# Optimization experiments

Measured on AMD Instinct MI355X. Metric: run time of the kernel, lower is better.

The kernel has to match this reference:

```python
import jax, jax.numpy as jnp
import numpy as np

THETA = 10000.0


def apply_rope(t):
    """Partial rotary on first head_dim//2 dims, interleaved pairs (rotary_embedding_torch).
    t: (B, H, S, D) float32."""
    B, H, S, D = t.shape
    rot_dim = D // 2  # RotaryEmbedding(head_dim // 2)
    inv_freq = 1.0 / (THETA ** (jnp.arange(0, rot_dim, 2, dtype=jnp.float32) / rot_dim))  # (rot_dim//2,)
    pos = jnp.arange(S, dtype=jnp.float32)
    freqs = pos[:, None] * inv_freq[None, :]            # (S, rot_dim//2)
    freqs = jnp.repeat(freqs, 2, axis=-1)               # (S, rot_dim) interleaved
    cos, sin = jnp.cos(freqs), jnp.sin(freqs)           # (S, rot_dim)
    t_rot, t_pass = t[..., :rot_dim], t[..., rot_dim:]
    x1 = t_rot[..., 0::2]
    x2 = t_rot[..., 1::2]
    rot_half = jnp.stack((-x2, x1), axis=-1).reshape(t_rot.shape)
    t_rot = t_rot * cos + rot_half * sin
    return jnp.concatenate([t_rot, t_pass], axis=-1)


def setup_inputs() -> dict:
    key = jax.random.key(0)
    k1, k2, k3, k4, k5 = jax.random.split(key, 5)
    B, S, Dm = 2, 2048, 1024
    scale = 1.0 / np.sqrt(Dm)
    return {
        "x": jax.random.normal(k1, (B, S, Dm), dtype=jnp.float32),
        "Wqkv": jax.random.normal(k2, (3 * Dm, Dm), dtype=jnp.float32) * scale,
        "bqkv": jax.random.normal(k3, (3 * Dm,), dtype=jnp.float32) * 0.01,
        "Wout": jax.random.normal(k4, (Dm, Dm), dtype=jnp.float32) * scale,
        "bout": jax.random.normal(k5, (Dm,), dtype=jnp.float32) * 0.01,
    }


def reference(x, Wqkv, bqkv, Wout, bout):
    B, S, Dm = x.shape
    H = 16
    Dh = Dm // H
    qkv = x @ Wqkv.T + bqkv                              # (B, S, 3*Dm)
    qkv = qkv.reshape(B, S, 3, H, Dh).transpose(2, 0, 3, 1, 4)  # (3, B, H, S, Dh)
    q, k, v = qkv[0], qkv[1], qkv[2]
    q = apply_rope(q.astype(jnp.float32))
    k = apply_rope(k.astype(jnp.float32))
    scores = jnp.einsum("bhqd,bhkd->bhqk", q, k) / jnp.sqrt(jnp.float32(Dh))
    attn = jax.nn.softmax(scores, axis=-1)
    out = jnp.einsum("bhqk,bhkd->bhqd", attn, v)         # (B, H, S, Dh)
    out = out.transpose(0, 2, 1, 3).reshape(B, S, Dm)
    return out @ Wout.T + bout
```

## Files before the change

### kernel.cpp

```cpp
#include <hip/hip_runtime.h>

#define S_LEN 2048
#define DMODEL 1024
#define NHEAD 16
#define DHEAD 64
#define BATCH 2
#define BH_TOT (BATCH * NHEAD)
#define TOK (BATCH * S_LEN)
#define NQKV (3 * DMODEL)

#define QSCALE 0.18033688011112042f

typedef float  f32x4  __attribute__((ext_vector_type(4)));
typedef float  f32x16 __attribute__((ext_vector_type(16)));
typedef int    i32x4  __attribute__((ext_vector_type(4)));
typedef __bf16 bf16x8 __attribute__((ext_vector_type(8)));
typedef __bf16 bf16x4 __attribute__((ext_vector_type(4)));
typedef __bf16 bf16x2 __attribute__((ext_vector_type(2)));

typedef __attribute__((address_space(1))) void* as1_ptr;
typedef __attribute__((address_space(3))) void* as3_ptr;

__device__ __forceinline__ void gl2lds16(const void* g, void* l) {
  __builtin_amdgcn_global_load_lds((as1_ptr)(void*)g, (as3_ptr)l, 16, 0, 0);
}

__device__ __forceinline__ f32x4 mfma32(bf16x8 a, bf16x8 b, f32x4 c) {
  return __builtin_amdgcn_mfma_f32_16x16x32_bf16(a, b, c, 0, 0, 0);
}

__device__ __forceinline__ f32x16 mfma3216(bf16x8 a, bf16x8 b, f32x16 c) {
  return __builtin_amdgcn_mfma_f32_32x32x16_bf16(a, b, c, 0, 0, 0);
}

__device__ __forceinline__ unsigned pack2(float a, float b) {
  bf16x2 t;
  t[0] = (__bf16)a;
  t[1] = (__bf16)b;
  return __builtin_bit_cast(unsigned, t);
}

__device__ __forceinline__ bf16x8 pfrag8(int hi,
                                         float a0, float a1, float a2, float a3,
                                         float a4, float a5, float a6, float a7) {
  const unsigned wA = pack2(a0, a1);
  const unsigned wB = pack2(a2, a3);
  const unsigned wC = pack2(a4, a5);
  const unsigned wD = pack2(a6, a7);
  const unsigned sA = (unsigned)__shfl_xor((int)wA, 32);
  const unsigned sB = (unsigned)__shfl_xor((int)wB, 32);
  const unsigned sC = (unsigned)__shfl_xor((int)wC, 32);
  const unsigned sD = (unsigned)__shfl_xor((int)wD, 32);
  const unsigned r0 = hi ? sC : wA;
  const unsigned r1 = hi ? sD : wB;
  const unsigned r2 = hi ? wC : sA;
  const unsigned r3 = hi ? wD : sB;
  const i32x4 w = {(int)r0, (int)r1, (int)r2, (int)r3};
  return __builtin_bit_cast(bf16x8, w);
}

__global__ __launch_bounds__(256) void cvt_kernel(const float* __restrict__ src,
                                                  __bf16* __restrict__ dst, int n) {
  const int i = (blockIdx.x * 256 + threadIdx.x) * 4;
  if (i >= n) return;
  const f32x4 v = *(const f32x4*)(src + i);
  bf16x4 o;
  o[0] = (__bf16)v[0]; o[1] = (__bf16)v[1]; o[2] = (__bf16)v[2]; o[3] = (__bf16)v[3];
  *(bf16x4*)(dst + i) = o;
}

__device__ __forceinline__ void gemm_tile_128(const __bf16* __restrict__ A,
                                              const __bf16* __restrict__ Bw,
                                              const int Kd, const int tileM, const int tileN,
                                              __bf16* As, __bf16* Bs, f32x4 acc[4][4]) {
  const int t    = threadIdx.x;
  const int lane = t & 63;
  const int wave = t >> 6;
  const int quad = lane >> 4;
  const int c    = lane & 15;
  const int wm   = (wave >> 1) << 6;
  const int wn   = (wave & 1) << 6;

  const int u0 = t, u1 = t + 256;
  const __bf16* gA0 = A  + (size_t)(tileM + (u0 >> 2)) * Kd + (u0 & 3) * 8;
  const __bf16* gA1 = A  + (size_t)(tileM + (u1 >> 2)) * Kd + (u1 & 3) * 8;
  const __bf16* gB0 = Bw + (size_t)(tileN + (u0 >> 2)) * Kd + (u0 & 3) * 8;
  const __bf16* gB1 = Bw + (size_t)(tileN + (u1 >> 2)) * Kd + (u1 & 3) * 8;
  __bf16* lA0 = As + u0 * 8; __bf16* lA1 = As + u1 * 8;
  __bf16* lB0 = Bs + u0 * 8; __bf16* lB1 = Bs + u1 * 8;

  for (int k0 = 0; k0 < Kd; k0 += 32) {
    gl2lds16(gA0 + k0, lA0);
    gl2lds16(gA1 + k0, lA1);
    gl2lds16(gB0 + k0, lB0);
    gl2lds16(gB1 + k0, lB1);
    __syncthreads();
    bf16x8 af[4], bfr[4];
#pragma unroll
    for (int mt = 0; mt < 4; ++mt)
      af[mt] = *(const bf16x8*)(As + (wm + mt * 16 + c) * 32 + quad * 8);
#pragma unroll
    for (int nt = 0; nt < 4; ++nt)
      bfr[nt] = *(const bf16x8*)(Bs + (wn + nt * 16 + c) * 32 + quad * 8);
#pragma unroll
    for (int mt = 0; mt < 4; ++mt)
#pragma unroll
      for (int nt = 0; nt < 4; ++nt)
        acc[mt][nt] = mfma32(af[mt], bfr[nt], acc[mt][nt]);
    __syncthreads();
  }
}

__global__ __launch_bounds__(256) void gemm_qkv_kernel(const __bf16* __restrict__ xb,
                                                       const __bf16* __restrict__ Wb,
                                                       const float* __restrict__ bias,
                                                       __bf16* __restrict__ Qb,
                                                       __bf16* __restrict__ Kb,
                                                       __bf16* __restrict__ Vtb) {
  __shared__ __align__(16) __bf16 As[128 * 32];
  __shared__ __align__(16) __bf16 Bs[128 * 32];
  f32x4 acc[4][4];
#pragma unroll
  for (int i = 0; i < 4; ++i)
#pragma unroll
    for (int j = 0; j < 4; ++j) acc[i][j] = (f32x4){0.f, 0.f, 0.f, 0.f};

  const int tileM = blockIdx.y * 128;
  const int tileN = blockIdx.x * 128;
  gemm_tile_128(xb, Wb, DMODEL, tileM, tileN, As, Bs, acc);

  const int t = threadIdx.x;
  const int lane = t & 63, wave = t >> 6;
  const int quad = lane >> 4, c = lane & 15;
  const int wm = (wave >> 1) << 6, wn = (wave & 1) << 6;

#pragma unroll
  for (int nt = 0; nt < 4; ++nt) {
    const int col = tileN + wn + nt * 16 + c;
    const float bv = bias[col];
    const int which = col >> 10;
    const int h  = (col >> 6) & 15;
    const int dh = col & 63;
    if (which == 2) {
#pragma unroll
      for (int mt = 0; mt < 4; ++mt) {
        const int row0 = tileM + wm + mt * 16 + quad * 4;
        const int bb = row0 >> 11;
        const int ss = row0 & (S_LEN - 1);
        bf16x4 o;
#pragma unroll
        for (int r = 0; r < 4; ++r) o[r] = (__bf16)(acc[mt][nt][r] + bv);
        *(bf16x4*)(Vtb + (((size_t)(bb * NHEAD + h)) * DHEAD + dh) * S_LEN + ss) = o;
      }
    } else {
      __bf16* dst = (which == 0) ? Qb : Kb;
      const float scl = (which == 0) ? QSCALE : 1.0f;
#pragma unroll
      for (int mt = 0; mt < 4; ++mt) {
#pragma unroll
        for (int r = 0; r < 4; ++r) {
          const int row = tileM + wm + mt * 16 + quad * 4 + r;
          const int bb = row >> 11;
          const int ss = row & (S_LEN - 1);
          dst[(((size_t)(bb * NHEAD + h)) * S_LEN + ss) * DHEAD + dh] =
              (__bf16)((acc[mt][nt][r] + bv) * scl);
        }
      }
    }
  }
}

__global__ __launch_bounds__(256) void gemm_out_kernel(const __bf16* __restrict__ AOb,
                                                       const __bf16* __restrict__ Wb,
                                                       const float* __restrict__ bout,
                                                       float* __restrict__ out) {
  __shared__ __align__(16) __bf16 As[128 * 32];
  __shared__ __align__(16) __bf16 Bs[128 * 32];
  f32x4 acc[4][4];
#pragma unroll
  for (int i = 0; i < 4; ++i)
#pragma unroll
    for (int j = 0; j < 4; ++j) acc[i][j] = (f32x4){0.f, 0.f, 0.f, 0.f};

  const int tileM = blockIdx.y * 128;
  const int tileN = blockIdx.x * 128;
  gemm_tile_128(AOb, Wb, DMODEL, tileM, tileN, As, Bs, acc);

  const int t = threadIdx.x;
  const int lane = t & 63, wave = t >> 6;
  const int quad = lane >> 4, c = lane & 15;
  const int wm = (wave >> 1) << 6, wn = (wave & 1) << 6;

#pragma unroll
  for (int nt = 0; nt < 4; ++nt) {
    const int col = tileN + wn + nt * 16 + c;
    const float bv = bout[col];
#pragma unroll
    for (int mt = 0; mt < 4; ++mt) {
#pragma unroll
      for (int r = 0; r < 4; ++r) {
        const int row = tileM + wm + mt * 16 + quad * 4 + r;
        out[(size_t)row * DMODEL + col] = acc[mt][nt][r] + bv;
      }
    }
  }
}

__global__ __launch_bounds__(256) void rope_kernel(__bf16* __restrict__ Qb, __bf16* __restrict__ Kb) {
  const int idx = blockIdx.x * 256 + threadIdx.x;
  const int j  = idx & 15;
  const int s  = (idx >> 4) & (S_LEN - 1);
  const int bh = (idx >> 15) & (BH_TOT - 1);
  __bf16* base = (idx >> 20) ? Kb : Qb;
  bf16x2* p = (bf16x2*)(base + ((size_t)bh * S_LEN + s) * DHEAD) + j;
  bf16x2 v = *p;
  const float x1 = (float)v[0];
  const float x2 = (float)v[1];
  const float LOG2_10000 = 13.287712379549449f;
  const float inv = exp2f(-(float)j * (LOG2_10000 / 16.0f));
  const float ang = (float)s * inv;
  float sn, cs;
  sincosf(ang, &sn, &cs);
  bf16x2 o;
  o[0] = (__bf16)(x1 * cs - x2 * sn);
  o[1] = (__bf16)(x2 * cs + x1 * sn);
  *p = o;
}

__global__ __launch_bounds__(256, 2) void attn_kernel(const __bf16* __restrict__ Qb,
                                                      const __bf16* __restrict__ Kb,
                                                      const __bf16* __restrict__ Vtb,
                                                      __bf16* __restrict__ AOb) {
  __shared__ __align__(16) __bf16 Ks[2][64 * 64];
  __shared__ __align__(16) __bf16 Vts[2][64 * 64];

  const int qt = blockIdx.x;
  const int bh = blockIdx.y;
  const int b = bh >> 4, h = bh & 15;
  const int t = threadIdx.x, wave = t >> 6, lane = t & 63;
  const int c31 = lane & 31, hi = lane >> 5;
  const int cx = c31 & 7;
  const size_t head = (size_t)bh * S_LEN * DHEAD;
  const int q0w = qt * 128 + wave * 32;

  bf16x8 qf[4];
#pragma unroll
  for (int s = 0; s < 4; ++s)
    qf[s] = *(const bf16x8*)(Qb + head + (size_t)(q0w + c31) * DHEAD + s * 16 + hi * 8);

  f32x16 zzero;
#pragma unroll
  for (int i = 0; i < 16; ++i) zzero[i] = 0.f;

  f32x16 ota[2], otb[2];
  ota[0] = zzero; ota[1] = zzero; otb[0] = zzero; otb[1] = zzero;
  float lp = 0.f;

  const int u0 = t, u1 = t + 256;
  const int r0 = u0 >> 3, ch0 = (u0 & 7) ^ (r0 & 7);
  const int r1 = u1 >> 3, ch1 = (u1 & 7) ^ (r1 & 7);
  const __bf16* kg0 = Kb + head + (size_t)r0 * DHEAD + ch0 * 8;
  const __bf16* kg1 = Kb + head + (size_t)r1 * DHEAD + ch1 * 8;
  const __bf16* vg0 = Vtb + ((size_t)bh * DHEAD + r0) * S_LEN + ch0 * 8;
  const __bf16* vg1 = Vtb + ((size_t)bh * DHEAD + r1) * S_LEN + ch1 * 8;

  gl2lds16(kg0, &Ks[0][u0 * 8]);
  gl2lds16(kg1, &Ks[0][u1 * 8]);
  gl2lds16(vg0, &Vts[0][u0 * 8]);
  gl2lds16(vg1, &Vts[0][u1 * 8]);

#define VREAD(db, gch) \
  (*(const bf16x8*)(&Vts[cur][((db) * 32 + c31) * 64 + ((((gch) + hi) ^ cx) * 8)]))

  for (int kb = 0; kb < S_LEN / 64; ++kb) {
    __syncthreads();
    const int cur = kb & 1;
    if (kb + 1 < S_LEN / 64) {
      const int nxt = cur ^ 1;
      const int k0n = (kb + 1) * 64;
      gl2lds16(kg0 + (size_t)k0n * DHEAD, &Ks[nxt][u0 * 8]);
      gl2lds16(kg1 + (size_t)k0n * DHEAD, &Ks[nxt][u1 * 8]);
      gl2lds16(vg0 + k0n, &Vts[nxt][u0 * 8]);
      gl2lds16(vg1 + k0n, &Vts[nxt][u1 * 8]);
    }

    bf16x8 kA0[4], kA1[4];
#pragma unroll
    for (int s = 0; s < 4; ++s) {
      kA0[s] = *(const bf16x8*)(&Ks[cur][c31 * 64 + (((s * 2 + hi) ^ cx) * 8)]);
      kA1[s] = *(const bf16x8*)(&Ks[cur][(32 + c31) * 64 + (((s * 2 + hi) ^ cx) * 8)]);
    }

    f32x16 z0 = zzero, z1 = zzero;
#pragma unroll
    for (int s = 0; s < 4; ++s) {
      z0 = mfma3216(kA0[s], qf[s], z0);
      z1 = mfma3216(kA1[s], qf[s], z1);
    }

    float p0[16], p1[16];
#pragma unroll
    for (int r = 0; r < 16; ++r) p0[r] = __builtin_amdgcn_exp2f(z0[r]);
#pragma unroll
    for (int r = 0; r < 16; ++r) p1[r] = __builtin_amdgcn_exp2f(z1[r]);

    lp += (((p0[0] + p0[1]) + (p0[2] + p0[3])) + ((p0[4] + p0[5]) + (p0[6] + p0[7])))
        + (((p0[8] + p0[9]) + (p0[10] + p0[11])) + ((p0[12] + p0[13]) + (p0[14] + p0[15])));
    lp += (((p1[0] + p1[1]) + (p1[2] + p1[3])) + ((p1[4] + p1[5]) + (p1[6] + p1[7])))
        + (((p1[8] + p1[9]) + (p1[10] + p1[11])) + ((p1[12] + p1[13]) + (p1[14] + p1[15])));

    {
      const bf16x8 f0 = pfrag8(hi, p0[0], p0[1], p0[2], p0[3], p0[4], p0[5], p0[6], p0[7]);
      ota[0] = mfma3216(VREAD(0, 0), f0, ota[0]);
      ota[1] = mfma3216(VREAD(1, 0), f0, ota[1]);
      const bf16x8 f1 = pfrag8(hi, p0[8], p0[9], p0[10], p0[11], p0[12], p0[13], p0[14], p0[15]);
      otb[0] = mfma3216(VREAD(0, 2), f1, otb[0]);
      otb[1] = mfma3216(VREAD(1, 2), f1, otb[1]);
    }
    {
      const bf16x8 f0 = pfrag8(hi, p1[0], p1[1], p1[2], p1[3], p1[4], p1[5], p1[6], p1[7]);
      ota[0] = mfma3216(VREAD(0, 4), f0, ota[0]);
      ota[1] = mfma3216(VREAD(1, 4), f0, ota[1]);
      const bf16x8 f1 = pfrag8(hi, p1[8], p1[9], p1[10], p1[11], p1[12], p1[13], p1[14], p1[15]);
      otb[0] = mfma3216(VREAD(0, 6), f1, otb[0]);
      otb[1] = mfma3216(VREAD(1, 6), f1, otb[1]);
    }
  }
#undef VREAD

#pragma unroll
  for (int i = 0; i < 16; ++i) { ota[0][i] += otb[0][i]; ota[1][i] += otb[1][i]; }
  const float l = lp + __shfl_xor(lp, 32);
  const float inv = 1.0f / l;
  const int q = q0w + c31;
#pragma unroll
  for (int db = 0; db < 2; ++db) {
#pragma unroll
    for (int rg = 0; rg < 4; ++rg) {
      bf16x4 o;
#pragma unroll
      for (int i = 0; i < 4; ++i) o[i] = (__bf16)(ota[db][rg * 4 + i] * inv);
      const int d0 = db * 32 + rg * 8 + hi * 4;
      *(bf16x4*)(AOb + ((size_t)(b * S_LEN + q)) * DMODEL + h * DHEAD + d0) = o;
    }
  }
}

extern "C" void kernel_launch(void* const* d_in, const int* in_sizes, int n_in,
                              void* d_out, int out_size, void* d_ws, size_t ws_size,
                              hipStream_t stream) {
  const float* x    = (const float*)d_in[0];
  const float* Wqkv = (const float*)d_in[1];
  const float* bqkv = (const float*)d_in[2];
  const float* Wout = (const float*)d_in[3];
  const float* bout = (const float*)d_in[4];
  float* out = (float*)d_out;

  char* ws = (char*)d_ws;
  __bf16* xb    = (__bf16*)(ws + 0);
  __bf16* Wqkvb = (__bf16*)(ws + (size_t)8  * 1024 * 1024);
  __bf16* Woutb = (__bf16*)(ws + (size_t)14 * 1024 * 1024);
  __bf16* Qb    = (__bf16*)(ws + (size_t)16 * 1024 * 1024);
  __bf16* Kb    = (__bf16*)(ws + (size_t)24 * 1024 * 1024);
  __bf16* Vtb   = (__bf16*)(ws + (size_t)32 * 1024 * 1024);
  __bf16* AOb   = (__bf16*)(ws + (size_t)40 * 1024 * 1024);

  cvt_kernel<<<(TOK * DMODEL) / 1024, 256, 0, stream>>>(x, xb, TOK * DMODEL);
  cvt_kernel<<<(NQKV * DMODEL) / 1024, 256, 0, stream>>>(Wqkv, Wqkvb, NQKV * DMODEL);
  cvt_kernel<<<(DMODEL * DMODEL) / 1024, 256, 0, stream>>>(Wout, Woutb, DMODEL * DMODEL);

  gemm_qkv_kernel<<<dim3(NQKV / 128, TOK / 128), 256, 0, stream>>>(xb, Wqkvb, bqkv, Qb, Kb, Vtb);

  rope_kernel<<<(2 * BH_TOT * S_LEN * 16) / 256, 256, 0, stream>>>(Qb, Kb);

  attn_kernel<<<dim3(S_LEN / 128, BH_TOT), 256, 0, stream>>>(Qb, Kb, Vtb, AOb);

  gemm_out_kernel<<<dim3(DMODEL / 128, TOK / 128), 256, 0, stream>>>(AOb, Woutb, bout, out);
}
```

Before: 204.5 us.

## Shrink attention blocks to two waves, drop P shuffles via permuted V reads, add setprio

The attention kernel now runs 128-thread blocks covering 64 queries, which doubles the grid and halves per-block K/V reuse, so each thread issues four async global-to-LDS loads per tile instead of two. The P-fragment construction no longer uses cross-half lane shuffles and selects. Instead, V^T is read from LDS as two 8-byte halves whose column order matches the natural P register layout. s_setprio is raised around the MFMA sections to favour matrix issue across waves. In exchange, K/V LDS traffic per query doubles and there are more LDS read instructions per MFMA.

```diff
diff --git a/kernel.cpp b/kernel.cpp
--- a/kernel.cpp
+++ b/kernel.cpp
@@ -14,6 +14,7 @@
 typedef float  f32x4  __attribute__((ext_vector_type(4)));
 typedef float  f32x16 __attribute__((ext_vector_type(16)));
 typedef int    i32x4  __attribute__((ext_vector_type(4)));
+typedef unsigned u32x2 __attribute__((ext_vector_type(2)));
 typedef __bf16 bf16x8 __attribute__((ext_vector_type(8)));
 typedef __bf16 bf16x4 __attribute__((ext_vector_type(4)));
 typedef __bf16 bf16x2 __attribute__((ext_vector_type(2)));
@@ -40,22 +41,10 @@
   return __builtin_bit_cast(unsigned, t);
 }
 
-__device__ __forceinline__ bf16x8 pfrag8(int hi,
-                                         float a0, float a1, float a2, float a3,
+__device__ __forceinline__ bf16x8 pfragn(float a0, float a1, float a2, float a3,
                                          float a4, float a5, float a6, float a7) {
-  const unsigned wA = pack2(a0, a1);
-  const unsigned wB = pack2(a2, a3);
-  const unsigned wC = pack2(a4, a5);
-  const unsigned wD = pack2(a6, a7);
-  const unsigned sA = (unsigned)__shfl_xor((int)wA, 32);
-  const unsigned sB = (unsigned)__shfl_xor((int)wB, 32);
-  const unsigned sC = (unsigned)__shfl_xor((int)wC, 32);
-  const unsigned sD = (unsigned)__shfl_xor((int)wD, 32);
-  const unsigned r0 = hi ? sC : wA;
-  const unsigned r1 = hi ? sD : wB;
-  const unsigned r2 = hi ? wC : sA;
-  const unsigned r3 = hi ? wD : sB;
-  const i32x4 w = {(int)r0, (int)r1, (int)r2, (int)r3};
+  const i32x4 w = {(int)pack2(a0, a1), (int)pack2(a2, a3),
+                   (int)pack2(a4, a5), (int)pack2(a6, a7)};
   return __builtin_bit_cast(bf16x8, w);
 }
 
@@ -227,7 +216,7 @@
   *p = o;
 }
 
-__global__ __launch_bounds__(256, 2) void attn_kernel(const __bf16* __restrict__ Qb,
+__global__ __launch_bounds__(128, 2) void attn_kernel(const __bf16* __restrict__ Qb,
                                                       const __bf16* __restrict__ Kb,
                                                       const __bf16* __restrict__ Vtb,
                                                       __bf16* __restrict__ AOb) {
@@ -241,7 +230,7 @@
   const int c31 = lane & 31, hi = lane >> 5;
   const int cx = c31 & 7;
   const size_t head = (size_t)bh * S_LEN * DHEAD;
-  const int q0w = qt * 128 + wave * 32;
+  const int q0w = qt * 64 + wave * 32;
 
   bf16x8 qf[4];
 #pragma unroll
@@ -256,21 +245,34 @@
   ota[0] = zzero; ota[1] = zzero; otb[0] = zzero; otb[1] = zzero;
   float lp = 0.f;
 
-  const int u0 = t, u1 = t + 256;
-  const int r0 = u0 >> 3, ch0 = (u0 & 7) ^ (r0 & 7);
-  const int r1 = u1 >> 3, ch1 = (u1 & 7) ^ (r1 & 7);
-  const __bf16* kg0 = Kb + head + (size_t)r0 * DHEAD + ch0 * 8;
-  const __bf16* kg1 = Kb + head + (size_t)r1 * DHEAD + ch1 * 8;
-  const __bf16* vg0 = Vtb + ((size_t)bh * DHEAD + r0) * S_LEN + ch0 * 8;
-  const __bf16* vg1 = Vtb + ((size_t)bh * DHEAD + r1) * S_LEN + ch1 * 8;
-
-  gl2lds16(kg0, &Ks[0][u0 * 8]);
-  gl2lds16(kg1, &Ks[0][u1 * 8]);
-  gl2lds16(vg0, &Vts[0][u0 * 8]);
-  gl2lds16(vg1, &Vts[0][u1 * 8]);
-
-#define VREAD(db, gch) \
-  (*(const bf16x8*)(&Vts[cur][((db) * 32 + c31) * 64 + ((((gch) + hi) ^ cx) * 8)]))
+  const __bf16* kg[4];
+  const __bf16* vg[4];
+  int loff[4];
+#pragma unroll
+  for (int i = 0; i < 4; ++i) {
+    const int u = t + 128 * i;
+    const int r = u >> 3, ch = (u & 7) ^ (r & 7);
+    kg[i] = Kb + head + (size_t)r * DHEAD + ch * 8;
+    vg[i] = Vtb + ((size_t)bh * DHEAD + r) * S_LEN + ch * 8;
+    loff[i] = u * 8;
+  }
+
+#pragma unroll
+  for (int i = 0; i < 4; ++i) {
+    gl2lds16(kg[i], &Ks[0][loff[i]]);
+    gl2lds16(vg[i], &Vts[0][loff[i]]);
+  }
+
+#define VREAD64(db, cb)                                                                   \
+  __builtin_bit_cast(bf16x8, (i32x4){                                                     \
+      (int)__builtin_bit_cast(u32x2, *(const bf16x4*)(&Vts[cur][((db)*32 + c31) * 64 +    \
+                                  (((cb) ^ cx) * 8) + hi * 4]))[0],                       \
+      (int)__builtin_bit_cast(u32x2, *(const bf16x4*)(&Vts[cur][((db)*32 + c31) * 64 +    \
+                                  (((cb) ^ cx) * 8) + hi * 4]))[1],                       \
+      (int)__builtin_bit_cast(u32x2, *(const bf16x4*)(&Vts[cur][((db)*32 + c31) * 64 +    \
+                                  ((((cb) + 1) ^ cx) * 8) + hi * 4]))[0],                 \
+      (int)__builtin_bit_cast(u32x2, *(const bf16x4*)(&Vts[cur][((db)*32 + c31) * 64 +    \
+                                  ((((cb) + 1) ^ cx) * 8) + hi * 4]))[1]})
 
   for (int kb = 0; kb < S_LEN / 64; ++kb) {
     __syncthreads();
@@ -278,10 +280,11 @@
     if (kb + 1 < S_LEN / 64) {
       const int nxt = cur ^ 1;
       const int k0n = (kb + 1) * 64;
-      gl2lds16(kg0 + (size_t)k0n * DHEAD, &Ks[nxt][u0 * 8]);
-      gl2lds16(kg1 + (size_t)k0n * DHEAD, &Ks[nxt][u1 * 8]);
-      gl2lds16(vg0 + k0n, &Vts[nxt][u0 * 8]);
-      gl2lds16(vg1 + k0n, &Vts[nxt][u1 * 8]);
+#pragma unroll
+      for (int i = 0; i < 4; ++i) {
+        gl2lds16(kg[i] + (size_t)k0n * DHEAD, &Ks[nxt][loff[i]]);
+        gl2lds16(vg[i] + k0n, &Vts[nxt][loff[i]]);
+      }
     }
 
     bf16x8 kA0[4], kA1[4];
@@ -292,11 +295,13 @@
     }
 
     f32x16 z0 = zzero, z1 = zzero;
+    __builtin_amdgcn_s_setprio(1);
 #pragma unroll
     for (int s = 0; s < 4; ++s) {
       z0 = mfma3216(kA0[s], qf[s], z0);
       z1 = mfma3216(kA1[s], qf[s], z1);
     }
+    __builtin_amdgcn_s_setprio(0);
 
     float p0[16], p1[16];
 #pragma unroll
@@ -309,24 +314,26 @@
     lp += (((p1[0] + p1[1]) + (p1[2] + p1[3])) + ((p1[4] + p1[5]) + (p1[6] + p1[7])))
         + (((p1[8] + p1[9]) + (p1[10] + p1[11])) + ((p1[12] + p1[13]) + (p1[14] + p1[15])));
 
+    __builtin_amdgcn_s_setprio(1);
     {
-      const bf16x8 f0 = pfrag8(hi, p0[0], p0[1], p0[2], p0[3], p0[4], p0[5], p0[6], p0[7]);
-      ota[0] = mfma3216(VREAD(0, 0), f0, ota[0]);
-      ota[1] = mfma3216(VREAD(1, 0), f0, ota[1]);
-      const bf16x8 f1 = pfrag8(hi, p0[8], p0[9], p0[10], p0[11], p0[12], p0[13], p0[14], p0[15]);
-      otb[0] = mfma3216(VREAD(0, 2), f1, otb[0]);
-      otb[1] = mfma3216(VREAD(1, 2), f1, otb[1]);
+      const bf16x8 f0 = pfragn(p0[0], p0[1], p0[2], p0[3], p0[4], p0[5], p0[6], p0[7]);
+      ota[0] = mfma3216(VREAD64(0, 0), f0, ota[0]);
+      ota[1] = mfma3216(VREAD64(1, 0), f0, ota[1]);
+      const bf16x8 f1 = pfragn(p0[8], p0[9], p0[10], p0[11], p0[12], p0[13], p0[14], p0[15]);
+      otb[0] = mfma3216(VREAD64(0, 2), f1, otb[0]);
+      otb[1] = mfma3216(VREAD64(1, 2), f1, otb[1]);
     }
     {
-      const bf16x8 f0 = pfrag8(hi, p1[0], p1[1], p1[2], p1[3], p1[4], p1[5], p1[6], p1[7]);
-      ota[0] = mfma3216(VREAD(0, 4), f0, ota[0]);
-      ota[1] = mfma3216(VREAD(1, 4), f0, ota[1]);
-      const bf16x8 f1 = pfrag8(hi, p1[8], p1[9], p1[10], p1[11], p1[12], p1[13], p1[14], p1[15]);
-      otb[0] = mfma3216(VREAD(0, 6), f1, otb[0]);
-      otb[1] = mfma3216(VREAD(1, 6), f1, otb[1]);
-    }
-  }
-#undef VREAD
+      const bf16x8 f0 = pfragn(p1[0], p1[1], p1[2], p1[3], p1[4], p1[5], p1[6], p1[7]);
+      ota[0] = mfma3216(VREAD64(0, 4), f0, ota[0]);
+      ota[1] = mfma3216(VREAD64(1, 4), f0, ota[1]);
+      const bf16x8 f1 = pfragn(p1[8], p1[9], p1[10], p1[11], p1[12], p1[13], p1[14], p1[15]);
+      otb[0] = mfma3216(VREAD64(0, 6), f1, otb[0]);
+      otb[1] = mfma3216(VREAD64(1, 6), f1, otb[1]);
+    }
+    __builtin_amdgcn_s_setprio(0);
+  }
+#undef VREAD64
 
 #pragma unroll
   for (int i = 0; i < 16; ++i) { ota[0][i] += otb[0][i]; ota[1][i] += otb[1][i]; }
@@ -373,7 +380,7 @@
 
   rope_kernel<<<(2 * BH_TOT * S_LEN * 16) / 256, 256, 0, stream>>>(Qb, Kb);
 
-  attn_kernel<<<dim3(S_LEN / 128, BH_TOT), 256, 0, stream>>>(Qb, Kb, Vtb, AOb);
+  attn_kernel<<<dim3(S_LEN / 64, BH_TOT), 128, 0, stream>>>(Qb, Kb, Vtb, AOb);
 
   gemm_out_kernel<<<dim3(DMODEL / 128, TOK / 128), 256, 0, stream>>>(AOb, Woutb, bout, out);
 }
```

Result: faster. 200.1 us (-2.2%).
